# Performance work log

Hardware: AMD Instinct MI355X
Metric: run time of the kernel (lower is better)

## Reference

```python
import jax, jax.numpy as jnp
import numpy as np

N = 100000
E = 1600000
IN_FEATS = 512
HIDDEN = 128
NUM_CLASSES = 2


def setup_inputs() -> dict:
    key = jax.random.key(0)
    k1, k2, k3, k4, k5, k6, k7 = jax.random.split(key, 7)
    inputs = jax.random.normal(k1, (N, IN_FEATS), dtype=jnp.float32)
    src = jax.random.randint(k2, (E,), 0, N, dtype=jnp.int64)
    dst = jax.random.randint(k3, (E,), 0, N, dtype=jnp.int64)
    # Glorot-style init like DGL GraphConv
    s1 = (6.0 / (IN_FEATS + HIDDEN)) ** 0.5
    s2 = (6.0 / (HIDDEN + NUM_CLASSES)) ** 0.5
    W1 = jax.random.uniform(k4, (IN_FEATS, HIDDEN), jnp.float32, -s1, s1)
    b1 = jnp.zeros((HIDDEN,), jnp.float32)
    W2 = jax.random.uniform(k5, (HIDDEN, NUM_CLASSES), jnp.float32, -s2, s2)
    b2 = jnp.zeros((NUM_CLASSES,), jnp.float32)
    return {"inputs": inputs, "W1": W1, "b1": b1, "W2": W2, "b2": b2,
            "src": src, "dst": dst}


def _graph_conv(x, W, b, src, dst, norm_src, norm_dst):
    # DGL GraphConv, norm='both': D_dst^{-1/2} A D_src^{-1/2} X W + b
    xw = x @ W                                   # [N, out] dense GEMM first (in >= out)
    m = (xw * norm_src[:, None])[src]            # gather messages [E, out]
    agg = jax.ops.segment_sum(m, dst, num_segments=N)  # scatter-add [N, out]
    return agg * norm_dst[:, None] + b


def reference(inputs, W1, b1, W2, b2, src, dst):
    ones = jnp.ones((src.shape[0],), jnp.float32)
    out_deg = jax.ops.segment_sum(ones, src, num_segments=N)
    in_deg = jax.ops.segment_sum(ones, dst, num_segments=N)
    norm_src = jax.lax.rsqrt(jnp.maximum(out_deg, 1.0))
    norm_dst = jax.lax.rsqrt(jnp.maximum(in_deg, 1.0))

    h = _graph_conv(inputs, W1, b1, src, dst, norm_src, norm_dst)
    h = jax.nn.relu(h)
    # dropout is identity at inference (training=False)
    h = _graph_conv(h, W2, b2, src, dst, norm_src, norm_dst)
    return jax.nn.softmax(h, axis=1)
```

## Files before the change

### kernel.cpp

```cpp
#include <hip/hip_runtime.h>
#include <math.h>

#define N_NODES 100000
#define N_EDGES 1600000
#define IN_F    512
#define HID     128

#define SH      8
#define NPB     256
#define BINS    ((N_NODES + NPB - 1) / NPB)
#define CBLK    256
#define EPB     ((N_EDGES + CBLK - 1) / CBLK)

typedef __attribute__((ext_vector_type(8))) _Float16 half8;
typedef __attribute__((ext_vector_type(2))) _Float16 half2v;
typedef __attribute__((ext_vector_type(4))) float float4v;

__global__ __launch_bounds__(256) void hist_kernel(const int* __restrict__ src,
                                                   const int* __restrict__ dst,
                                                   int* __restrict__ dbh, int* __restrict__ sbh) {
    __shared__ int hd[BINS], hs[BINS];
    const int t = threadIdx.x, blk = blockIdx.x;
    for (int i = t; i < BINS; i += 256) { hd[i] = 0; hs[i] = 0; }
    __syncthreads();
    const int e0 = blk * EPB, e1 = min(N_EDGES, e0 + EPB);
    for (int e = e0 + t; e < e1; e += 256) {
        atomicAdd(&hd[dst[e] >> SH], 1);
        atomicAdd(&hs[src[e] >> SH], 1);
    }
    __syncthreads();
    for (int i = t; i < BINS; i += 256) {
        dbh[i * CBLK + blk] = hd[i];
        sbh[i * CBLK + blk] = hs[i];
    }
}

__global__ __launch_bounds__(256) void binscan_kernel(int* __restrict__ dbh, int* __restrict__ sbh,
                                                      int* __restrict__ dtot, int* __restrict__ stot) {
    __shared__ int sh[256];
    const int b = blockIdx.x, t = threadIdx.x;
    int* arr; int* tot;
    if (b < BINS) { arr = dbh + (size_t)b * CBLK; tot = &dtot[b]; }
    else          { arr = sbh + (size_t)(b - BINS) * CBLK; tot = &stot[b - BINS]; }
    int v = arr[t];
    sh[t] = v; __syncthreads();
#pragma unroll
    for (int d = 1; d < 256; d <<= 1) {
        int u = (t >= d) ? sh[t - d] : 0;
        __syncthreads();
        sh[t] += u;
        __syncthreads();
    }
    arr[t] = sh[t] - v;
    if (t == 255) *tot = sh[255];
}

__global__ __launch_bounds__(512) void binbase_kernel(const int* __restrict__ dtot,
                                                      const int* __restrict__ stot,
                                                      int* __restrict__ dbase, int* __restrict__ sbase,
                                                      int* __restrict__ offs) {
    __shared__ int sh[512];
    const int t = threadIdx.x;
    int v = (t < BINS) ? dtot[t] : 0;
    sh[t] = v; __syncthreads();
#pragma unroll
    for (int d = 1; d < 512; d <<= 1) {
        int u = (t >= d) ? sh[t - d] : 0;
        __syncthreads();
        sh[t] += u;
        __syncthreads();
    }
    if (t < BINS) dbase[t] = sh[t] - v;
    if (t == BINS - 1) { dbase[BINS] = sh[t]; offs[N_NODES] = sh[t]; }
    __syncthreads();
    int v2 = (t < BINS) ? stot[t] : 0;
    sh[t] = v2; __syncthreads();
#pragma unroll
    for (int d = 1; d < 512; d <<= 1) {
        int u = (t >= d) ? sh[t - d] : 0;
        __syncthreads();
        sh[t] += u;
        __syncthreads();
    }
    if (t < BINS) sbase[t] = sh[t] - v2;
    if (t == BINS - 1) sbase[BINS] = sh[t];
}

__global__ __launch_bounds__(256) void scatter_bins_kernel(const int* __restrict__ src,
                                                           const int* __restrict__ dst,
                                                           const int* __restrict__ dbh,
                                                           const int* __restrict__ sbh,
                                                           const int* __restrict__ dbase,
                                                           const int* __restrict__ sbase,
                                                           int* __restrict__ ds_dst,
                                                           int* __restrict__ ds_src,
                                                           int* __restrict__ ss_src) {
    __shared__ int dcur[BINS], scur[BINS];
    const int t = threadIdx.x, blk = blockIdx.x;
    for (int i = t; i < BINS; i += 256) {
        dcur[i] = dbase[i] + dbh[i * CBLK + blk];
        scur[i] = sbase[i] + sbh[i * CBLK + blk];
    }
    __syncthreads();
    const int e0 = blk * EPB, e1 = min(N_EDGES, e0 + EPB);
    for (int e = e0 + t; e < e1; e += 256) {
        int d = dst[e], s = src[e];
        int p = atomicAdd(&dcur[d >> SH], 1);
        ds_dst[p] = d; ds_src[p] = s;
        int q = atomicAdd(&scur[s >> SH], 1);
        ss_src[q] = s;
    }
}

__global__ __launch_bounds__(256) void finalize_kernel(const int* __restrict__ ds_dst,
                                                       const int* __restrict__ ds_src,
                                                       const int* __restrict__ ss_src,
                                                       const int* __restrict__ dbase,
                                                       const int* __restrict__ sbase,
                                                       int* __restrict__ csr, int* __restrict__ offs,
                                                       float* __restrict__ norm_dst,
                                                       float* __restrict__ norm_src) {
    __shared__ int cnt[NPB], pos[NPB];
    const int t = threadIdx.x, b = blockIdx.x;
    if (b < BINS) {
        const int start = dbase[b], end = dbase[b + 1];
        cnt[t] = 0; __syncthreads();
        for (int k = start + t; k < end; k += 256)
            atomicAdd(&cnt[ds_dst[k] & (NPB - 1)], 1);
        __syncthreads();
        const int c = cnt[t];
        pos[t] = c; __syncthreads();
#pragma unroll
        for (int d = 1; d < 256; d <<= 1) {
            int u = (t >= d) ? pos[t - d] : 0;
            __syncthreads();
            pos[t] += u;
            __syncthreads();
        }
        const int excl = pos[t] - c;
        const int node = (b << SH) + t;
        if (node < N_NODES) {
            offs[node] = start + excl;
            norm_dst[node] = rsqrtf(fmaxf((float)c, 1.0f));
        }
        cnt[t] = start + excl;
        __syncthreads();
        for (int k = start + t; k < end; k += 256) {
            int dl = ds_dst[k] & (NPB - 1);
            int p = atomicAdd(&cnt[dl], 1);
            csr[p] = ds_src[k];
        }
    } else {
        const int bb = b - BINS;
        const int start = sbase[bb], end = sbase[bb + 1];
        cnt[t] = 0; __syncthreads();
        for (int k = start + t; k < end; k += 256)
            atomicAdd(&cnt[ss_src[k] & (NPB - 1)], 1);
        __syncthreads();
        const int node = (bb << SH) + t;
        if (node < N_NODES)
            norm_src[node] = rsqrtf(fmaxf((float)cnt[t], 1.0f));
    }
}

__global__ void cvtW1_kernel(const float* __restrict__ W1, _Float16* __restrict__ W1T) {
    int i = blockIdx.x * blockDim.x + threadIdx.x;
    if (i < IN_F * HID) {
        int k = i >> 7, c = i & 127;
        W1T[(size_t)c * IN_F + k] = (_Float16)W1[i];
    }
}

#define APAD 40
__global__ __launch_bounds__(256) void gemm1_mfma_kernel(const float* __restrict__ X,
                                                         const _Float16* __restrict__ W1T,
                                                         const float* __restrict__ norm_src,
                                                         _Float16* __restrict__ xwh) {
    __shared__ _Float16 As[2][128 * APAD];

    const int t    = threadIdx.x;
    const int wave = t >> 6;
    const int lane = t & 63;
    const int m0   = blockIdx.x * 128;
    const int quad = lane >> 4;
    const int l16  = lane & 15;

    float4v acc[2][8];
#pragma unroll
    for (int r = 0; r < 2; r++)
#pragma unroll
        for (int c = 0; c < 8; c++) acc[r][c] = (float4v)0.f;

    const int srow = t >> 1;
    const int sc16 = (t & 1) * 16;
    const int sgrow = m0 + srow;
    const bool svalid = sgrow < N_NODES;
    const float* xbase = X + (size_t)sgrow * IN_F + sc16;

    float4 va[4];
#pragma unroll
    for (int i = 0; i < 4; i++) va[i] = make_float4(0.f, 0.f, 0.f, 0.f);
    if (svalid) {
        const float4* xp = reinterpret_cast<const float4*>(xbase);
        va[0] = xp[0]; va[1] = xp[1]; va[2] = xp[2]; va[3] = xp[3];
    }
    half8 bfrag[8];
#pragma unroll
    for (int ct = 0; ct < 8; ct++)
        bfrag[ct] = *reinterpret_cast<const half8*>(&W1T[(size_t)(ct * 16 + l16) * IN_F + quad * 8]);

    {
        half8 h0, h1;
        h0[0]=(_Float16)va[0].x; h0[1]=(_Float16)va[0].y; h0[2]=(_Float16)va[0].z; h0[3]=(_Float16)va[0].w;
        h0[4]=(_Float16)va[1].x; h0[5]=(_Float16)va[1].y; h0[6]=(_Float16)va[1].z; h0[7]=(_Float16)va[1].w;
        h1[0]=(_Float16)va[2].x; h1[1]=(_Float16)va[2].y; h1[2]=(_Float16)va[2].z; h1[3]=(_Float16)va[2].w;
        h1[4]=(_Float16)va[3].x; h1[5]=(_Float16)va[3].y; h1[6]=(_Float16)va[3].z; h1[7]=(_Float16)va[3].w;
        *reinterpret_cast<half8*>(&As[0][srow * APAD + sc16 + 0]) = h0;
        *reinterpret_cast<half8*>(&As[0][srow * APAD + sc16 + 8]) = h1;
    }

    int cur = 0;
    for (int it = 0; it < IN_F / 32; it++) {
        const int ktn = (it + 1) * 32;
        const bool more = ktn < IN_F;
        __syncthreads();

        float4 vb[4];
        half8 bnext[8];
        if (more) {
            if (svalid) {
                const float4* xp = reinterpret_cast<const float4*>(xbase + ktn);
                vb[0] = xp[0]; vb[1] = xp[1]; vb[2] = xp[2]; vb[3] = xp[3];
            } else {
                vb[0] = vb[1] = vb[2] = vb[3] = make_float4(0.f, 0.f, 0.f, 0.f);
            }
#pragma unroll
            for (int ct = 0; ct < 8; ct++)
                bnext[ct] = *reinterpret_cast<const half8*>(
                    &W1T[(size_t)(ct * 16 + l16) * IN_F + ktn + quad * 8]);
        }

        half8 afrag[2];
#pragma unroll
        for (int r = 0; r < 2; r++)
            afrag[r] = *reinterpret_cast<const half8*>(
                &As[cur][(wave * 32 + r * 16 + l16) * APAD + quad * 8]);
#pragma unroll
        for (int r = 0; r < 2; r++)
#pragma unroll
            for (int ct = 0; ct < 8; ct++)
                acc[r][ct] = __builtin_amdgcn_mfma_f32_16x16x32_f16(afrag[r], bfrag[ct], acc[r][ct], 0, 0, 0);

        if (more) {
            half8 h0, h1;
            h0[0]=(_Float16)vb[0].x; h0[1]=(_Float16)vb[0].y; h0[2]=(_Float16)vb[0].z; h0[3]=(_Float16)vb[0].w;
            h0[4]=(_Float16)vb[1].x; h0[5]=(_Float16)vb[1].y; h0[6]=(_Float16)vb[1].z; h0[7]=(_Float16)vb[1].w;
            h1[0]=(_Float16)vb[2].x; h1[1]=(_Float16)vb[2].y; h1[2]=(_Float16)vb[2].z; h1[3]=(_Float16)vb[2].w;
            h1[4]=(_Float16)vb[3].x; h1[5]=(_Float16)vb[3].y; h1[6]=(_Float16)vb[3].z; h1[7]=(_Float16)vb[3].w;
            *reinterpret_cast<half8*>(&As[cur ^ 1][srow * APAD + sc16 + 0]) = h0;
            *reinterpret_cast<half8*>(&As[cur ^ 1][srow * APAD + sc16 + 8]) = h1;
#pragma unroll
            for (int ct = 0; ct < 8; ct++) bfrag[ct] = bnext[ct];
        }
        cur ^= 1;
    }

#pragma unroll
    for (int r = 0; r < 2; r++) {
#pragma unroll
        for (int i = 0; i < 4; i++) {
            int grow = m0 + wave * 32 + r * 16 + quad * 4 + i;
            if (grow < N_NODES) {
                float s = norm_src[grow];
                _Float16* orow = &xwh[(size_t)grow * HID];
#pragma unroll
                for (int ct = 0; ct < 8; ct++)
                    orow[ct * 16 + l16] = (_Float16)(acc[r][ct][i] * s);
            }
        }
    }
}

__global__ __launch_bounds__(256) void gather1_kernel(
        const int* __restrict__ csr, const int* __restrict__ offs,
        const _Float16* __restrict__ xwh, const float* __restrict__ norm_dst,
        const float* __restrict__ norm_src, const float* __restrict__ b1,
        const float* __restrict__ W2, float* __restrict__ hw2) {
    const int w    = (blockIdx.x * blockDim.x + threadIdx.x) >> 6;
    const int lane = threadIdx.x & 63;
    if (w >= N_NODES) return;
    const int off = offs[w], end = offs[w + 1];
    const int j2 = lane * 2;

    float a0 = 0.f, a1 = 0.f;
    int k = off;
    for (; k + 4 <= end; k += 4) {
        int s0 = csr[k], s1 = csr[k + 1], s2 = csr[k + 2], s3 = csr[k + 3];
        half2v v0 = *reinterpret_cast<const half2v*>(&xwh[(size_t)s0 * HID + j2]);
        half2v v1 = *reinterpret_cast<const half2v*>(&xwh[(size_t)s1 * HID + j2]);
        half2v v2 = *reinterpret_cast<const half2v*>(&xwh[(size_t)s2 * HID + j2]);
        half2v v3 = *reinterpret_cast<const half2v*>(&xwh[(size_t)s3 * HID + j2]);
        a0 += (float)v0[0] + (float)v1[0] + (float)v2[0] + (float)v3[0];
        a1 += (float)v0[1] + (float)v1[1] + (float)v2[1] + (float)v3[1];
    }
    for (; k < end; k++) {
        half2v v = *reinterpret_cast<const half2v*>(&xwh[(size_t)csr[k] * HID + j2]);
        a0 += (float)v[0]; a1 += (float)v[1];
    }

    const float nd = norm_dst[w];
    float2 b = *reinterpret_cast<const float2*>(&b1[j2]);
    float h0 = fmaxf(a0 * nd + b.x, 0.f);
    float h1 = fmaxf(a1 * nd + b.y, 0.f);
    float2 w2a = reinterpret_cast<const float2*>(W2)[j2];
    float2 w2b = reinterpret_cast<const float2*>(W2)[j2 + 1];
    float p0 = h0 * w2a.x + h1 * w2b.x;
    float p1 = h0 * w2a.y + h1 * w2b.y;
#pragma unroll
    for (int offd = 32; offd > 0; offd >>= 1) {
        p0 += __shfl_down(p0, offd);
        p1 += __shfl_down(p1, offd);
    }
    if (lane == 0) {
        float ns = norm_src[w];
        reinterpret_cast<float2*>(hw2)[w] = make_float2(p0 * ns, p1 * ns);
    }
}

__global__ void gather2_softmax_kernel(
        const int* __restrict__ csr, const int* __restrict__ offs,
        const float* __restrict__ hw2, const float* __restrict__ norm_dst,
        const float* __restrict__ b2, float* __restrict__ out) {
    const int w    = (blockIdx.x * blockDim.x + threadIdx.x) >> 6;
    const int lane = threadIdx.x & 63;
    const int sub  = lane >> 4, k0 = lane & 15;
    const int n = w * 4 + sub;
    if (n >= N_NODES) return;
    const int off = offs[n], end = offs[n + 1];

    float a0 = 0.f, a1 = 0.f;
    for (int k = off + k0; k < end; k += 16) {
        int s = csr[k];
        float2 v = reinterpret_cast<const float2*>(hw2)[s];
        a0 += v.x; a1 += v.y;
    }
#pragma unroll
    for (int d = 1; d < 16; d <<= 1) {
        a0 += __shfl_xor(a0, d);
        a1 += __shfl_xor(a1, d);
    }
    if (k0 == 0) {
        float nd = norm_dst[n];
        float z0 = a0 * nd + b2[0];
        float z1 = a1 * nd + b2[1];
        float m = fmaxf(z0, z1);
        float e0 = expf(z0 - m), e1 = expf(z1 - m);
        float inv = 1.f / (e0 + e1);
        reinterpret_cast<float2*>(out)[n] = make_float2(e0 * inv, e1 * inv);
    }
}

extern "C" void kernel_launch(void* const* d_in, const int* in_sizes, int n_in,
                              void* d_out, int out_size, void* d_ws, size_t ws_size,
                              hipStream_t stream) {
    const float* X   = (const float*)d_in[0];
    const float* W1  = (const float*)d_in[1];
    const float* b1  = (const float*)d_in[2];
    const float* W2  = (const float*)d_in[3];
    const float* b2  = (const float*)d_in[4];
    const int*   src = (const int*)d_in[5];
    const int*   dst = (const int*)d_in[6];
    float* out = (float*)d_out;

    const size_t N = N_NODES;
    char* ws = (char*)d_ws;
    int*   dbh      = (int*)ws;   ws += (size_t)BINS * CBLK * 4;
    int*   sbh      = (int*)ws;   ws += (size_t)BINS * CBLK * 4;
    int*   dtot     = (int*)ws;   ws += BINS * 4;
    int*   stot     = (int*)ws;   ws += BINS * 4;
    int*   dbase    = (int*)ws;   ws += (BINS + 1) * 4;
    int*   sbase    = (int*)ws;   ws += (BINS + 1) * 4;
    int*   ds_dst   = (int*)ws;   ws += (size_t)N_EDGES * 4;
    int*   ds_src   = (int*)ws;   ws += (size_t)N_EDGES * 4;
    int*   ss_src   = (int*)ws;   ws += (size_t)N_EDGES * 4;
    int*   csr      = (int*)ws;   ws += (size_t)N_EDGES * 4;
    int*   offs     = (int*)ws;   ws += (N + 1) * 4;
    float* norm_src = (float*)ws; ws += N * 4;
    float* norm_dst = (float*)ws; ws += N * 4;
    float* hw2      = (float*)ws; ws += N * 2 * 4;
    _Float16* W1T   = (_Float16*)ws; ws += (size_t)IN_F * HID * 2;
    _Float16* xwh   = (_Float16*)ws; ws += N * (size_t)HID * 2;

    hist_kernel<<<CBLK, 256, 0, stream>>>(src, dst, dbh, sbh);
    binscan_kernel<<<2 * BINS, 256, 0, stream>>>(dbh, sbh, dtot, stot);
    binbase_kernel<<<1, 512, 0, stream>>>(dtot, stot, dbase, sbase, offs);
    scatter_bins_kernel<<<CBLK, 256, 0, stream>>>(src, dst, dbh, sbh, dbase, sbase,
                                                  ds_dst, ds_src, ss_src);
    finalize_kernel<<<2 * BINS, 256, 0, stream>>>(ds_dst, ds_src, ss_src, dbase, sbase,
                                                  csr, offs, norm_dst, norm_src);
    cvtW1_kernel<<<(IN_F * HID + 255) / 256, 256, 0, stream>>>(W1, W1T);
    gemm1_mfma_kernel<<<(N_NODES + 127) / 128, 256, 0, stream>>>(X, W1T, norm_src, xwh);
    gather1_kernel<<<(N_NODES * 64 + 255) / 256, 256, 0, stream>>>(
        csr, offs, xwh, norm_dst, norm_src, b1, W2, hw2);
    gather2_softmax_kernel<<<(((int)N + 3) / 4 * 64 + 255) / 256, 256, 0, stream>>>(
        csr, offs, hw2, norm_dst, b2, out);
}
```

Measured before the change: 523.6 us.

## Load GEMM1 A fragments directly to registers and widen gather1 loads to half8

The GEMM1 kernel drops the LDS double-buffer staging of X and has each lane load its MFMA A-fragment straight from global memory into registers, prefetched one K-step ahead. This removes the LDS writes, reads and per-iteration barriers. The cost is less coalesced global loads, since each lane reads 32 bytes per row. The gather1 kernel now splits each wave into four sub-groups that process different edges in parallel with 16-byte half8 loads, then combines them with cross-lane shuffles. This gives more memory-level parallelism per node.

```diff
diff --git a/kernel.cpp b/kernel.cpp
--- a/kernel.cpp
+++ b/kernel.cpp
@@ -13,7 +13,6 @@
 #define EPB     ((N_EDGES + CBLK - 1) / CBLK)
 
 typedef __attribute__((ext_vector_type(8))) _Float16 half8;
-typedef __attribute__((ext_vector_type(2))) _Float16 half2v;
 typedef __attribute__((ext_vector_type(4))) float float4v;
 
 __global__ __launch_bounds__(256) void hist_kernel(const int* __restrict__ src,
@@ -171,19 +170,24 @@
     }
 }
 
-#define APAD 40
 __global__ __launch_bounds__(256) void gemm1_mfma_kernel(const float* __restrict__ X,
                                                          const _Float16* __restrict__ W1T,
                                                          const float* __restrict__ norm_src,
                                                          _Float16* __restrict__ xwh) {
-    __shared__ _Float16 As[2][128 * APAD];
-
     const int t    = threadIdx.x;
     const int wave = t >> 6;
     const int lane = t & 63;
-    const int m0   = blockIdx.x * 128;
     const int quad = lane >> 4;
     const int l16  = lane & 15;
+    const int m0   = blockIdx.x * 128;
+
+    const int row0 = m0 + wave * 32 + l16;
+    const int row1 = row0 + 16;
+    const bool val0 = row0 < N_NODES;
+    const bool val1 = row1 < N_NODES;
+    const float* xp0 = X + (size_t)row0 * IN_F + quad * 8;
+    const float* xp1 = X + (size_t)row1 * IN_F + quad * 8;
+    const _Float16* wp = W1T + quad * 8 + (size_t)l16 * IN_F;
 
     float4v acc[2][8];
 #pragma unroll
@@ -191,78 +195,51 @@
 #pragma unroll
         for (int c = 0; c < 8; c++) acc[r][c] = (float4v)0.f;
 
-    const int srow = t >> 1;
-    const int sc16 = (t & 1) * 16;
-    const int sgrow = m0 + srow;
-    const bool svalid = sgrow < N_NODES;
-    const float* xbase = X + (size_t)sgrow * IN_F + sc16;
-
-    float4 va[4];
-#pragma unroll
-    for (int i = 0; i < 4; i++) va[i] = make_float4(0.f, 0.f, 0.f, 0.f);
-    if (svalid) {
-        const float4* xp = reinterpret_cast<const float4*>(xbase);
-        va[0] = xp[0]; va[1] = xp[1]; va[2] = xp[2]; va[3] = xp[3];
-    }
-    half8 bfrag[8];
+    const float4 fz = make_float4(0.f, 0.f, 0.f, 0.f);
+
+    float4 nA[2][2];
+    half8  nB[8];
+
+    nA[0][0] = val0 ? reinterpret_cast<const float4*>(xp0)[0] : fz;
+    nA[0][1] = val0 ? reinterpret_cast<const float4*>(xp0)[1] : fz;
+    nA[1][0] = val1 ? reinterpret_cast<const float4*>(xp1)[0] : fz;
+    nA[1][1] = val1 ? reinterpret_cast<const float4*>(xp1)[1] : fz;
 #pragma unroll
     for (int ct = 0; ct < 8; ct++)
-        bfrag[ct] = *reinterpret_cast<const half8*>(&W1T[(size_t)(ct * 16 + l16) * IN_F + quad * 8]);
-
-    {
-        half8 h0, h1;
-        h0[0]=(_Float16)va[0].x; h0[1]=(_Float16)va[0].y; h0[2]=(_Float16)va[0].z; h0[3]=(_Float16)va[0].w;
-        h0[4]=(_Float16)va[1].x; h0[5]=(_Float16)va[1].y; h0[6]=(_Float16)va[1].z; h0[7]=(_Float16)va[1].w;
-        h1[0]=(_Float16)va[2].x; h1[1]=(_Float16)va[2].y; h1[2]=(_Float16)va[2].z; h1[3]=(_Float16)va[2].w;
-        h1[4]=(_Float16)va[3].x; h1[5]=(_Float16)va[3].y; h1[6]=(_Float16)va[3].z; h1[7]=(_Float16)va[3].w;
-        *reinterpret_cast<half8*>(&As[0][srow * APAD + sc16 + 0]) = h0;
-        *reinterpret_cast<half8*>(&As[0][srow * APAD + sc16 + 8]) = h1;
-    }
-
-    int cur = 0;
+        nB[ct] = *reinterpret_cast<const half8*>(wp + (size_t)ct * 16 * IN_F);
+
     for (int it = 0; it < IN_F / 32; it++) {
-        const int ktn = (it + 1) * 32;
-        const bool more = ktn < IN_F;
-        __syncthreads();
-
-        float4 vb[4];
-        half8 bnext[8];
-        if (more) {
-            if (svalid) {
-                const float4* xp = reinterpret_cast<const float4*>(xbase + ktn);
-                vb[0] = xp[0]; vb[1] = xp[1]; vb[2] = xp[2]; vb[3] = xp[3];
-            } else {
-                vb[0] = vb[1] = vb[2] = vb[3] = make_float4(0.f, 0.f, 0.f, 0.f);
-            }
+        float4 cA[2][2];
+        half8  cB[8];
+#pragma unroll
+        for (int r = 0; r < 2; r++) { cA[r][0] = nA[r][0]; cA[r][1] = nA[r][1]; }
+#pragma unroll
+        for (int ct = 0; ct < 8; ct++) cB[ct] = nB[ct];
+
+        if (it + 1 < IN_F / 32) {
+            const int kt = (it + 1) * 32;
+            nA[0][0] = val0 ? reinterpret_cast<const float4*>(xp0 + kt)[0] : fz;
+            nA[0][1] = val0 ? reinterpret_cast<const float4*>(xp0 + kt)[1] : fz;
+            nA[1][0] = val1 ? reinterpret_cast<const float4*>(xp1 + kt)[0] : fz;
+            nA[1][1] = val1 ? reinterpret_cast<const float4*>(xp1 + kt)[1] : fz;
 #pragma unroll
             for (int ct = 0; ct < 8; ct++)
-                bnext[ct] = *reinterpret_cast<const half8*>(
-                    &W1T[(size_t)(ct * 16 + l16) * IN_F + ktn + quad * 8]);
-        }
-
-        half8 afrag[2];
+                nB[ct] = *reinterpret_cast<const half8*>(wp + kt + (size_t)ct * 16 * IN_F);
+        }
+
+        half8 af[2];
+#pragma unroll
+        for (int r = 0; r < 2; r++) {
+            af[r][0] = (_Float16)cA[r][0].x; af[r][1] = (_Float16)cA[r][0].y;
+            af[r][2] = (_Float16)cA[r][0].z; af[r][3] = (_Float16)cA[r][0].w;
+            af[r][4] = (_Float16)cA[r][1].x; af[r][5] = (_Float16)cA[r][1].y;
+            af[r][6] = (_Float16)cA[r][1].z; af[r][7] = (_Float16)cA[r][1].w;
+        }
 #pragma unroll
         for (int r = 0; r < 2; r++)
-            afrag[r] = *reinterpret_cast<const half8*>(
-                &As[cur][(wave * 32 + r * 16 + l16) * APAD + quad * 8]);
-#pragma unroll
-        for (int r = 0; r < 2; r++)
 #pragma unroll
             for (int ct = 0; ct < 8; ct++)
-                acc[r][ct] = __builtin_amdgcn_mfma_f32_16x16x32_f16(afrag[r], bfrag[ct], acc[r][ct], 0, 0, 0);
-
-        if (more) {
-            half8 h0, h1;
-            h0[0]=(_Float16)vb[0].x; h0[1]=(_Float16)vb[0].y; h0[2]=(_Float16)vb[0].z; h0[3]=(_Float16)vb[0].w;
-            h0[4]=(_Float16)vb[1].x; h0[5]=(_Float16)vb[1].y; h0[6]=(_Float16)vb[1].z; h0[7]=(_Float16)vb[1].w;
-            h1[0]=(_Float16)vb[2].x; h1[1]=(_Float16)vb[2].y; h1[2]=(_Float16)vb[2].z; h1[3]=(_Float16)vb[2].w;
-            h1[4]=(_Float16)vb[3].x; h1[5]=(_Float16)vb[3].y; h1[6]=(_Float16)vb[3].z; h1[7]=(_Float16)vb[3].w;
-            *reinterpret_cast<half8*>(&As[cur ^ 1][srow * APAD + sc16 + 0]) = h0;
-            *reinterpret_cast<half8*>(&As[cur ^ 1][srow * APAD + sc16 + 8]) = h1;
-#pragma unroll
-            for (int ct = 0; ct < 8; ct++) bfrag[ct] = bnext[ct];
-        }
-        cur ^= 1;
+                acc[r][ct] = __builtin_amdgcn_mfma_f32_16x16x32_f16(af[r], cB[ct], acc[r][ct], 0, 0, 0);
     }
 
 #pragma unroll
@@ -289,37 +266,42 @@
     const int w    = (blockIdx.x * blockDim.x + threadIdx.x) >> 6;
     const int lane = threadIdx.x & 63;
     if (w >= N_NODES) return;
+    const int sub = lane >> 4, j16 = lane & 15;
     const int off = offs[w], end = offs[w + 1];
-    const int j2 = lane * 2;
-
-    float a0 = 0.f, a1 = 0.f;
-    int k = off;
-    for (; k + 4 <= end; k += 4) {
-        int s0 = csr[k], s1 = csr[k + 1], s2 = csr[k + 2], s3 = csr[k + 3];
-        half2v v0 = *reinterpret_cast<const half2v*>(&xwh[(size_t)s0 * HID + j2]);
-        half2v v1 = *reinterpret_cast<const half2v*>(&xwh[(size_t)s1 * HID + j2]);
-        half2v v2 = *reinterpret_cast<const half2v*>(&xwh[(size_t)s2 * HID + j2]);
-        half2v v3 = *reinterpret_cast<const half2v*>(&xwh[(size_t)s3 * HID + j2]);
-        a0 += (float)v0[0] + (float)v1[0] + (float)v2[0] + (float)v3[0];
-        a1 += (float)v0[1] + (float)v1[1] + (float)v2[1] + (float)v3[1];
-    }
-    for (; k < end; k++) {
-        half2v v = *reinterpret_cast<const half2v*>(&xwh[(size_t)csr[k] * HID + j2]);
-        a0 += (float)v[0]; a1 += (float)v[1];
+
+    float acc[8];
+#pragma unroll
+    for (int i = 0; i < 8; i++) acc[i] = 0.f;
+
+    for (int k = off + sub; k < end; k += 4) {
+        int s = csr[k];
+        half8 v = *reinterpret_cast<const half8*>(&xwh[(size_t)s * HID + j16 * 8]);
+#pragma unroll
+        for (int i = 0; i < 8; i++) acc[i] += (float)v[i];
+    }
+#pragma unroll
+    for (int i = 0; i < 8; i++) {
+        acc[i] += __shfl_xor(acc[i], 16);
+        acc[i] += __shfl_xor(acc[i], 32);
     }
 
     const float nd = norm_dst[w];
-    float2 b = *reinterpret_cast<const float2*>(&b1[j2]);
-    float h0 = fmaxf(a0 * nd + b.x, 0.f);
-    float h1 = fmaxf(a1 * nd + b.y, 0.f);
-    float2 w2a = reinterpret_cast<const float2*>(W2)[j2];
-    float2 w2b = reinterpret_cast<const float2*>(W2)[j2 + 1];
-    float p0 = h0 * w2a.x + h1 * w2b.x;
-    float p1 = h0 * w2a.y + h1 * w2b.y;
-#pragma unroll
-    for (int offd = 32; offd > 0; offd >>= 1) {
-        p0 += __shfl_down(p0, offd);
-        p1 += __shfl_down(p1, offd);
+    float4 b1a = reinterpret_cast<const float4*>(b1)[j16 * 2];
+    float4 b1b = reinterpret_cast<const float4*>(b1)[j16 * 2 + 1];
+    float bb[8] = {b1a.x, b1a.y, b1a.z, b1a.w, b1b.x, b1b.y, b1b.z, b1b.w};
+
+    float p0 = 0.f, p1 = 0.f;
+#pragma unroll
+    for (int i = 0; i < 8; i++) {
+        float h = fmaxf(acc[i] * nd + bb[i], 0.f);
+        float2 w2 = reinterpret_cast<const float2*>(W2)[j16 * 8 + i];
+        p0 += h * w2.x;
+        p1 += h * w2.y;
+    }
+#pragma unroll
+    for (int d = 1; d < 16; d <<= 1) {
+        p0 += __shfl_xor(p0, d);
+        p1 += __shfl_xor(p1, d);
     }
     if (lane == 0) {
         float ns = norm_src[w];
```

New measurement: 612.3 us. 16.9% more time.
